# Optimization experiments

Hardware: AMD Instinct MI355X
Metric: run time of the kernel (lower is better)

The kernel has to match this reference:

```python
import jax, jax.numpy as jnp
import numpy as np

N_CON, N_VAR, E, D = 100000, 200000, 1600000, 128


def setup_inputs() -> dict:
    key = jax.random.key(0)
    ks = jax.random.split(key, 10)
    s = 1.0 / np.sqrt(D)
    return {
        "x_con": jax.random.normal(ks[0], (N_CON, D), jnp.float32),
        "x_var": jax.random.normal(ks[1], (N_VAR, D), jnp.float32),
        "e_con": jax.random.randint(ks[2], (E,), 0, N_CON, jnp.int32),
        "e_var": jax.random.randint(ks[3], (E,), 0, N_VAR, jnp.int32),
        # GraphConv for edge type constraint->variable (updates variable nodes)
        "W_rel_cv": jax.random.normal(ks[4], (D, D), jnp.float32) * s,
        "b_cv": jnp.zeros((D,), jnp.float32),
        "W_root_cv": jax.random.normal(ks[5], (D, D), jnp.float32) * s,
        # GraphConv for edge type variable->constraint (updates constraint nodes)
        "W_rel_vc": jax.random.normal(ks[6], (D, D), jnp.float32) * s,
        "b_vc": jnp.zeros((D,), jnp.float32),
        "W_root_vc": jax.random.normal(ks[7], (D, D), jnp.float32) * s,
        # per-node-type LayerNorm params
        "ln_g_con": jnp.ones((D,), jnp.float32),
        "ln_b_con": jnp.zeros((D,), jnp.float32),
        "ln_g_var": jnp.ones((D,), jnp.float32),
        "ln_b_var": jnp.zeros((D,), jnp.float32),
    }


def _layer_norm(x, g, b, eps=1e-5):
    m = jnp.mean(x, axis=-1, keepdims=True)
    v = jnp.var(x, axis=-1, keepdims=True)
    return (x - m) * jax.lax.rsqrt(v + eps) * g + b


def reference(x_con, x_var, e_con, e_var,
              W_rel_cv, b_cv, W_root_cv,
              W_rel_vc, b_vc, W_root_vc,
              ln_g_con, ln_b_con, ln_g_var, ln_b_var):
    # GraphConv (aggr='add'): out = lin_rel(sum_j x_j) + lin_root(x_dst)
    # constraint -> variable: gather constraint feats, scatter-add onto variables
    agg_var = jax.ops.segment_sum(x_con[e_con], e_var, num_segments=N_VAR)  # [N_VAR, D]
    out_var = agg_var @ W_rel_cv + b_cv + x_var @ W_root_cv
    # variable -> constraint (reverse edges)
    agg_con = jax.ops.segment_sum(x_var[e_var], e_con, num_segments=N_CON)  # [N_CON, D]
    out_con = agg_con @ W_rel_vc + b_vc + x_con @ W_root_vc
    # LayerNorm + ReLU per node type
    out_con = jax.nn.relu(_layer_norm(out_con, ln_g_con, ln_b_con))
    out_var = jax.nn.relu(_layer_norm(out_var, ln_g_var, ln_b_var))
    return out_con, out_var
```

## Files before the change

### kernel.cpp

```cpp
#include <hip/hip_runtime.h>
#include <hip/hip_bf16.h>
#include <hip/hip_fp16.h>

#define DD 128

typedef __attribute__((ext_vector_type(8))) short bf8;
typedef __attribute__((ext_vector_type(4))) float f32x4;

__device__ __forceinline__ ushort f2bf(float x) {
    return __bfloat16_as_ushort(__float2bfloat16(x));
}
__device__ __forceinline__ float bf2f(ushort h) {
    return __uint_as_float(((unsigned)h) << 16);
}

__global__ __launch_bounds__(256)
void to_fp16(const float* __restrict__ in, __half* __restrict__ out, long n)
{
    long i = ((long)blockIdx.x * 256 + threadIdx.x) * 8;
    if (i >= n) return;
    float4 a = *(const float4*)(in + i);
    float4 b = *(const float4*)(in + i + 4);
    __half2 h0 = __floats2half2_rn(a.x, a.y);
    __half2 h1 = __floats2half2_rn(a.z, a.w);
    __half2 h2 = __floats2half2_rn(b.x, b.y);
    __half2 h3 = __floats2half2_rn(b.z, b.w);
    uint4 o;
    o.x = *(unsigned*)&h0; o.y = *(unsigned*)&h1;
    o.z = *(unsigned*)&h2; o.w = *(unsigned*)&h3;
    *(uint4*)(out + i) = o;
}

#define NBMAX 640
#define CAP 16384

__global__ __launch_bounds__(256)
void bucket_hist(const int* __restrict__ e_con, const int* __restrict__ e_var,
                 int* __restrict__ btot, int N_CON, int NT, int E)
{
    __shared__ int cnt[NBMAX];
    const int NB = (NT + 511) >> 9;
    const int tid = threadIdx.x;
    for (int b = tid; b < NB; b += 256) cnt[b] = 0;
    __syncthreads();
    long e0 = (long)blockIdx.x * 4096;
#pragma unroll
    for (int i = 0; i < 16; ++i) {
        long e = e0 + i * 256 + tid;
        if (e < E) {
            atomicAdd(&cnt[e_con[e] >> 9], 1);
            atomicAdd(&cnt[(N_CON + e_var[e]) >> 9], 1);
        }
    }
    __syncthreads();
    for (int b = tid; b < NB; b += 256)
        if (cnt[b]) atomicAdd(&btot[b], cnt[b]);
}

__global__ __launch_bounds__(1024)
void bucket_scan(const int* __restrict__ btot, int* __restrict__ gbase,
                 int* __restrict__ gcursor, int NB)
{
    const int tid = threadIdx.x, lane = tid & 63, wave = tid >> 6;
    int v = (tid < NB) ? btot[tid] : 0;
    int x = v;
#pragma unroll
    for (int d = 1; d < 64; d <<= 1) {
        int y = __shfl_up(x, d);
        if (lane >= d) x += y;
    }
    __shared__ int wt[16];
    if (lane == 63) wt[wave] = x;
    __syncthreads();
    int off = 0;
    for (int w = 0; w < wave; ++w) off += wt[w];
    int excl = x - v + off;
    if (tid < NB) { gbase[tid] = excl; gcursor[tid] = excl; }
    if (tid == NB - 1) gbase[NB] = excl + v;
}

__global__ __launch_bounds__(256)
void binA(const int* __restrict__ e_con, const int* __restrict__ e_var,
          int* __restrict__ gcursor, unsigned* __restrict__ staging,
          int N_CON, int NT, int E)
{
    __shared__ int cnt[NBMAX], base[NBMAX];
    const int NB = (NT + 511) >> 9;
    const int tid = threadIdx.x;
    for (int b = tid; b < NB; b += 256) cnt[b] = 0;
    __syncthreads();
    long e0 = (long)blockIdx.x * 4096;
    int cs[16], vs[16];
#pragma unroll
    for (int i = 0; i < 16; ++i) {
        long e = e0 + i * 256 + tid;
        bool ok = e < E;
        cs[i] = ok ? e_con[e] : -1;
        vs[i] = ok ? e_var[e] : 0;
    }
#pragma unroll
    for (int i = 0; i < 16; ++i) if (cs[i] >= 0) {
        atomicAdd(&cnt[cs[i] >> 9], 1);
        atomicAdd(&cnt[(N_CON + vs[i]) >> 9], 1);
    }
    __syncthreads();
    for (int b = tid; b < NB; b += 256) {
        int c = cnt[b];
        base[b] = c ? atomicAdd(&gcursor[b], c) : 0;
        cnt[b] = 0;
    }
    __syncthreads();
#pragma unroll
    for (int i = 0; i < 16; ++i) if (cs[i] >= 0) {
        int d1 = cs[i];
        int p1 = base[d1 >> 9] + atomicAdd(&cnt[d1 >> 9], 1);
        staging[p1] = ((unsigned)(d1 & 511) << 18) | (unsigned)vs[i];
        int d2 = N_CON + vs[i];
        int p2 = base[d2 >> 9] + atomicAdd(&cnt[d2 >> 9], 1);
        staging[p2] = ((unsigned)(d2 & 511) << 18) | (unsigned)cs[i];
    }
}

__global__ __launch_bounds__(256)
void bucket_sort(const unsigned* __restrict__ staging, const int* __restrict__ gbase,
                 int* __restrict__ row_ptr, int* __restrict__ srclist, int NT)
{
    __shared__ int dcnt[512], dbase[512], wt[4];
    __shared__ unsigned srcbuf[CAP];
    const int b = blockIdx.x, tid = threadIdx.x;
    const int nbase = gbase[b];
    int n = gbase[b + 1] - nbase;
    if (n > CAP) n = CAP;

    for (int i = tid; i < 512; i += 256) dcnt[i] = 0;
    __syncthreads();
    for (int i = tid; i < n; i += 256)
        atomicAdd(&dcnt[staging[nbase + i] >> 18], 1);
    __syncthreads();

    int c0 = dcnt[2 * tid], c1 = dcnt[2 * tid + 1];
    int ts = c0 + c1, x = ts;
#pragma unroll
    for (int d = 1; d < 64; d <<= 1) {
        int y = __shfl_up(x, d);
        if ((tid & 63) >= d) x += y;
    }
    if ((tid & 63) == 63) wt[tid >> 6] = x;
    __syncthreads();
    int woff = 0;
    for (int w = 0; w < (tid >> 6); ++w) woff += wt[w];
    int ex = x - ts + woff;
    dbase[2 * tid] = ex;
    dbase[2 * tid + 1] = ex + c0;
    int nd = (b << 9) + 2 * tid;
    if (nd < NT)     row_ptr[nd]     = nbase + ex;
    if (nd + 1 < NT) row_ptr[nd + 1] = nbase + ex + c0;
    __syncthreads();

    for (int i = tid; i < 512; i += 256) dcnt[i] = 0;
    __syncthreads();
    for (int i = tid; i < n; i += 256) {
        unsigned e = staging[nbase + i];
        int d = e >> 18;
        int pos = dbase[d] + atomicAdd(&dcnt[d], 1);
        srcbuf[pos] = e & 0x3FFFFu;
    }
    __syncthreads();
    for (int i = tid; i < n; i += 256)
        srclist[nbase + i] = (int)srcbuf[i];
}

__global__ __launch_bounds__(256)
void gather_kernel(const __half2* __restrict__ hc, const __half2* __restrict__ hv,
                   const int* __restrict__ row_ptr, const int* __restrict__ srclist,
                   float* __restrict__ out, int N_CON, int NT, int twoE)
{
    int n = blockIdx.x * 4 + (threadIdx.x >> 6);
    if (n >= NT) return;
    int lane = threadIdx.x & 63;
    int start = row_ptr[n];
    int end = (n + 1 < NT) ? row_ptr[n + 1] : twoE;
    const __half2* src = (n < N_CON) ? hv : hc;

    float2 a0 = make_float2(0.f, 0.f);
    float2 a1 = make_float2(0.f, 0.f);
    int j = start;
    for (; j + 8 <= end; j += 8) {
        int i0 = srclist[j + 0], i1 = srclist[j + 1];
        int i2 = srclist[j + 2], i3 = srclist[j + 3];
        int i4 = srclist[j + 4], i5 = srclist[j + 5];
        int i6 = srclist[j + 6], i7 = srclist[j + 7];
        float2 t0 = __half22float2(src[(long)i0 * 64 + lane]);
        float2 t1 = __half22float2(src[(long)i1 * 64 + lane]);
        float2 t2 = __half22float2(src[(long)i2 * 64 + lane]);
        float2 t3 = __half22float2(src[(long)i3 * 64 + lane]);
        float2 t4 = __half22float2(src[(long)i4 * 64 + lane]);
        float2 t5 = __half22float2(src[(long)i5 * 64 + lane]);
        float2 t6 = __half22float2(src[(long)i6 * 64 + lane]);
        float2 t7 = __half22float2(src[(long)i7 * 64 + lane]);
        a0.x += (t0.x + t1.x) + (t2.x + t3.x);
        a0.y += (t0.y + t1.y) + (t2.y + t3.y);
        a1.x += (t4.x + t5.x) + (t6.x + t7.x);
        a1.y += (t4.y + t5.y) + (t6.y + t7.y);
    }
    if (j + 4 <= end) {
        int i0 = srclist[j + 0], i1 = srclist[j + 1];
        int i2 = srclist[j + 2], i3 = srclist[j + 3];
        float2 t0 = __half22float2(src[(long)i0 * 64 + lane]);
        float2 t1 = __half22float2(src[(long)i1 * 64 + lane]);
        float2 t2 = __half22float2(src[(long)i2 * 64 + lane]);
        float2 t3 = __half22float2(src[(long)i3 * 64 + lane]);
        a0.x += (t0.x + t1.x) + (t2.x + t3.x);
        a0.y += (t0.y + t1.y) + (t2.y + t3.y);
        j += 4;
    }
    if (j + 2 <= end) {
        int i0 = srclist[j + 0], i1 = srclist[j + 1];
        float2 t0 = __half22float2(src[(long)i0 * 64 + lane]);
        float2 t1 = __half22float2(src[(long)i1 * 64 + lane]);
        a1.x += t0.x + t1.x;
        a1.y += t0.y + t1.y;
        j += 2;
    }
    if (j < end) {
        float2 t0 = __half22float2(src[(long)srclist[j] * 64 + lane]);
        a0.x += t0.x;
        a0.y += t0.y;
    }
    a0.x += a1.x; a0.y += a1.y;
    ((float2*)(out + (long)n * DD))[lane] = a0;
}

__global__ __launch_bounds__(512, 4)
void gemm_mfma_ln(const float* __restrict__ agg, const float* __restrict__ xroot,
                  const float* __restrict__ Wrel, const float* __restrict__ Wroot,
                  const float* __restrict__ bias,
                  const float* __restrict__ ln_g, const float* __restrict__ ln_b,
                  float* __restrict__ out, int M)
{
    __shared__ ushort Blds[2 * 8192];

    const int wid  = threadIdx.x >> 6;
    const int lane = threadIdx.x & 63;
    const int lq   = lane >> 4;
    const int lc   = lane & 15;
    const long wrow0 = (long)blockIdx.x * 256 + wid * 32;

    const float* ap[2]; const float* xp[2];
#pragma unroll
    for (int rt = 0; rt < 2; ++rt) {
        long rr = wrow0 + rt * 16 + lc;
        if (rr >= M) rr = 0;
        ap[rt] = agg   + rr * DD;
        xp[rt] = xroot + rr * DD;
    }

    f32x4 acc[2][8] = {};

    for (int c = 0; c < 4; ++c) {
        const float* W = (c < 2) ? Wrel : Wroot;
        const int krow0 = (c & 1) * 8;
        __syncthreads();
        for (int g = threadIdx.x; g < 1024; g += 512) {
            int krl = g >> 7, col = g & 127;
            const float* wp = W + (long)(krow0 + krl) * 8 * DD + col;
            bf8 vh, vl;
#pragma unroll
            for (int j = 0; j < 8; ++j) {
                float w = wp[(long)j * DD];
                ushort h = f2bf(w);
                vh[j] = (short)h;
                vl[j] = (short)f2bf(w - bf2f(h));
            }
            int base = (g * 8) ^ ((krl & 3) << 3);
            *(bf8*)&Blds[base] = vh;
            *(bf8*)&Blds[8192 + base] = vl;
        }
        __syncthreads();

#pragma unroll
        for (int ks2 = 0; ks2 < 2; ++ks2) {
            const int ks = c * 2 + ks2;
            const int kk0 = ks * 32;
            bf8 ah[2], al[2];
#pragma unroll
            for (int rt = 0; rt < 2; ++rt) {
                const float* rp = (ks < 4) ? ap[rt] : xp[rt];
                const int koff  = (ks < 4) ? kk0 : (kk0 - 128);
                const float4* p = (const float4*)(rp + koff + lq * 8);
                float4 f0 = p[0], f1 = p[1];
                float v[8] = {f0.x, f0.y, f0.z, f0.w, f1.x, f1.y, f1.z, f1.w};
#pragma unroll
                for (int j = 0; j < 8; ++j) {
                    ushort h = f2bf(v[j]);
                    ah[rt][j] = (short)h;
                    al[rt][j] = (short)f2bf(v[j] - bf2f(h));
                }
            }
            const int krl0 = ks2 * 4 + lq;
#pragma unroll
            for (int colt = 0; colt < 8; ++colt) {
                int off = ((krl0 * 128 + colt * 16 + lc) * 8) ^ (lq << 3);
                bf8 bh = *(const bf8*)&Blds[off];
                bf8 bl = *(const bf8*)&Blds[8192 + off];
#pragma unroll
                for (int rt = 0; rt < 2; ++rt) {
                    acc[rt][colt] = __builtin_amdgcn_mfma_f32_16x16x32_bf16(ah[rt], bh, acc[rt][colt], 0, 0, 0);
                    acc[rt][colt] = __builtin_amdgcn_mfma_f32_16x16x32_bf16(ah[rt], bl, acc[rt][colt], 0, 0, 0);
                    acc[rt][colt] = __builtin_amdgcn_mfma_f32_16x16x32_bf16(al[rt], bh, acc[rt][colt], 0, 0, 0);
                }
            }
        }
    }

    float biasv[8], gv[8], bv[8];
#pragma unroll
    for (int colt = 0; colt < 8; ++colt) {
        int col = colt * 16 + lc;
        biasv[colt] = bias[col]; gv[colt] = ln_g[col]; bv[colt] = ln_b[col];
    }
#pragma unroll
    for (int rt = 0; rt < 2; ++rt) {
#pragma unroll
        for (int r = 0; r < 4; ++r) {
            long row = wrow0 + rt * 16 + lq * 4 + r;
            float v[8];
            float s = 0.f;
#pragma unroll
            for (int colt = 0; colt < 8; ++colt) { v[colt] = acc[rt][colt][r] + biasv[colt]; s += v[colt]; }
#pragma unroll
            for (int m = 8; m >= 1; m >>= 1) s += __shfl_xor(s, m);
            float mean = s * (1.0f / 128.0f);
            float vq = 0.f;
#pragma unroll
            for (int colt = 0; colt < 8; ++colt) { v[colt] -= mean; vq += v[colt] * v[colt]; }
#pragma unroll
            for (int m = 8; m >= 1; m >>= 1) vq += __shfl_xor(vq, m);
            float inv = rsqrtf(vq * (1.0f / 128.0f) + 1e-5f);
            if (row < M) {
#pragma unroll
                for (int colt = 0; colt < 8; ++colt) {
                    out[row * DD + colt * 16 + lc] =
                        fmaxf(fmaf(v[colt] * inv, gv[colt], bv[colt]), 0.f);
                }
            }
        }
    }
}

extern "C" void kernel_launch(void* const* d_in, const int* in_sizes, int n_in,
                              void* d_out, int out_size, void* d_ws, size_t ws_size,
                              hipStream_t stream)
{
    const float* x_con     = (const float*)d_in[0];
    const float* x_var     = (const float*)d_in[1];
    const int*   e_con     = (const int*)d_in[2];
    const int*   e_var     = (const int*)d_in[3];
    const float* W_rel_cv  = (const float*)d_in[4];
    const float* b_cv      = (const float*)d_in[5];
    const float* W_root_cv = (const float*)d_in[6];
    const float* W_rel_vc  = (const float*)d_in[7];
    const float* b_vc      = (const float*)d_in[8];
    const float* W_root_vc = (const float*)d_in[9];
    const float* ln_g_con  = (const float*)d_in[10];
    const float* ln_b_con  = (const float*)d_in[11];
    const float* ln_g_var  = (const float*)d_in[12];
    const float* ln_b_var  = (const float*)d_in[13];

    const int N_CON = in_sizes[0] / DD;
    const int N_VAR = in_sizes[1] / DD;
    const int E     = in_sizes[2];
    const int NT    = N_CON + N_VAR;
    const int twoE  = 2 * E;
    const int NB    = (NT + 511) >> 9;

    __half*   hxc     = (__half*)d_ws;
    __half*   hxv     = hxc + (size_t)N_CON * DD;
    int*      row_ptr = (int*)(hxv + (size_t)N_VAR * DD);
    int*      srclist = row_ptr + NT;
    unsigned* staging = (unsigned*)(srclist + twoE);
    int*      btot    = (int*)(staging + twoE);
    int*      gbase   = btot + NB;
    int*      gcursor = gbase + NB + 1;

    float* out_all = (float*)d_out;

    const int eb4 = (E + 4095) / 4096;
    const long nc_elems = (long)N_CON * DD, nv_elems = (long)N_VAR * DD;

    hipMemsetAsync(btot, 0, (size_t)NB * sizeof(int), stream);
    to_fp16<<<(int)((nc_elems / 8 + 255) / 256), 256, 0, stream>>>(x_con, hxc, nc_elems);
    to_fp16<<<(int)((nv_elems / 8 + 255) / 256), 256, 0, stream>>>(x_var, hxv, nv_elems);
    bucket_hist<<<eb4, 256, 0, stream>>>(e_con, e_var, btot, N_CON, NT, E);
    bucket_scan<<<1, 1024, 0, stream>>>(btot, gbase, gcursor, NB);
    binA<<<eb4, 256, 0, stream>>>(e_con, e_var, gcursor, staging, N_CON, NT, E);
    bucket_sort<<<NB, 256, 0, stream>>>(staging, gbase, row_ptr, srclist, NT);

    gather_kernel<<<(NT + 3) / 4, 256, 0, stream>>>((const __half2*)hxc, (const __half2*)hxv,
                                                    row_ptr, srclist,
                                                    out_all, N_CON, NT, twoE);

    gemm_mfma_ln<<<(N_CON + 255) / 256, 512, 0, stream>>>(
        out_all, x_con, W_rel_vc, W_root_vc, b_vc, ln_g_con, ln_b_con, out_all, N_CON);
    gemm_mfma_ln<<<(N_VAR + 255) / 256, 512, 0, stream>>>(
        out_all + (size_t)N_CON * DD, x_var, W_rel_cv, W_root_cv, b_cv,
        ln_g_var, ln_b_var, out_all + (size_t)N_CON * DD, N_VAR);
}
```

Measured before the change: 390.9 us.

## Drop histogram pass via fixed-capacity buckets; store aggregates as split bf16

Binning now writes edges into fixed-capacity per-bucket staging slots using a global cursor, so the separate histogram kernel goes away and the prefix scan runs after binning on the final counts. The gather kernel writes each aggregated row as pre-split bf16 high/low halves instead of fp32, so the GEMM loads MFMA operands directly and skips the conversion for the aggregate half of K. The staging buffer grows to NB*CAPS entries, and edges beyond the bucket capacity are dropped silently, which matches the existing clamp in bucket_sort.

```diff
diff --git a/kernel.cpp b/kernel.cpp
--- a/kernel.cpp
+++ b/kernel.cpp
@@ -3,6 +3,8 @@
 #include <hip/hip_fp16.h>
 
 #define DD 128
+#define CAPS 16384
+#define NBMAX 640
 
 typedef __attribute__((ext_vector_type(8))) short bf8;
 typedef __attribute__((ext_vector_type(4))) float f32x4;
@@ -31,53 +33,6 @@
     *(uint4*)(out + i) = o;
 }
 
-#define NBMAX 640
-#define CAP 16384
-
-__global__ __launch_bounds__(256)
-void bucket_hist(const int* __restrict__ e_con, const int* __restrict__ e_var,
-                 int* __restrict__ btot, int N_CON, int NT, int E)
-{
-    __shared__ int cnt[NBMAX];
-    const int NB = (NT + 511) >> 9;
-    const int tid = threadIdx.x;
-    for (int b = tid; b < NB; b += 256) cnt[b] = 0;
-    __syncthreads();
-    long e0 = (long)blockIdx.x * 4096;
-#pragma unroll
-    for (int i = 0; i < 16; ++i) {
-        long e = e0 + i * 256 + tid;
-        if (e < E) {
-            atomicAdd(&cnt[e_con[e] >> 9], 1);
-            atomicAdd(&cnt[(N_CON + e_var[e]) >> 9], 1);
-        }
-    }
-    __syncthreads();
-    for (int b = tid; b < NB; b += 256)
-        if (cnt[b]) atomicAdd(&btot[b], cnt[b]);
-}
-
-__global__ __launch_bounds__(1024)
-void bucket_scan(const int* __restrict__ btot, int* __restrict__ gbase,
-                 int* __restrict__ gcursor, int NB)
-{
-    const int tid = threadIdx.x, lane = tid & 63, wave = tid >> 6;
-    int v = (tid < NB) ? btot[tid] : 0;
-    int x = v;
-#pragma unroll
-    for (int d = 1; d < 64; d <<= 1) {
-        int y = __shfl_up(x, d);
-        if (lane >= d) x += y;
-    }
-    __shared__ int wt[16];
-    if (lane == 63) wt[wave] = x;
-    __syncthreads();
-    int off = 0;
-    for (int w = 0; w < wave; ++w) off += wt[w];
-    int excl = x - v + off;
-    if (tid < NB) { gbase[tid] = excl; gcursor[tid] = excl; }
-    if (tid == NB - 1) gbase[NB] = excl + v;
-}
 
 __global__ __launch_bounds__(256)
 void binA(const int* __restrict__ e_con, const int* __restrict__ e_var,
@@ -112,13 +67,36 @@
     __syncthreads();
 #pragma unroll
     for (int i = 0; i < 16; ++i) if (cs[i] >= 0) {
-        int d1 = cs[i];
-        int p1 = base[d1 >> 9] + atomicAdd(&cnt[d1 >> 9], 1);
-        staging[p1] = ((unsigned)(d1 & 511) << 18) | (unsigned)vs[i];
-        int d2 = N_CON + vs[i];
-        int p2 = base[d2 >> 9] + atomicAdd(&cnt[d2 >> 9], 1);
-        staging[p2] = ((unsigned)(d2 & 511) << 18) | (unsigned)cs[i];
-    }
+        int d1 = cs[i], b1 = d1 >> 9;
+        int p1 = base[b1] + atomicAdd(&cnt[b1], 1);
+        if (p1 < CAPS)
+            staging[(long)b1 * CAPS + p1] = ((unsigned)(d1 & 511) << 18) | (unsigned)vs[i];
+        int d2 = N_CON + vs[i], b2 = d2 >> 9;
+        int p2 = base[b2] + atomicAdd(&cnt[b2], 1);
+        if (p2 < CAPS)
+            staging[(long)b2 * CAPS + p2] = ((unsigned)(d2 & 511) << 18) | (unsigned)cs[i];
+    }
+}
+
+__global__ __launch_bounds__(1024)
+void bucket_scan(const int* __restrict__ btot, int* __restrict__ gbase, int NB)
+{
+    const int tid = threadIdx.x, lane = tid & 63, wave = tid >> 6;
+    int v = (tid < NB) ? btot[tid] : 0;
+    int x = v;
+#pragma unroll
+    for (int d = 1; d < 64; d <<= 1) {
+        int y = __shfl_up(x, d);
+        if (lane >= d) x += y;
+    }
+    __shared__ int wt[16];
+    if (lane == 63) wt[wave] = x;
+    __syncthreads();
+    int off = 0;
+    for (int w = 0; w < wave; ++w) off += wt[w];
+    int excl = x - v + off;
+    if (tid < NB) gbase[tid] = excl;
+    if (tid == NB - 1) gbase[NB] = excl + v;
 }
 
 __global__ __launch_bounds__(256)
@@ -126,16 +104,17 @@
                  int* __restrict__ row_ptr, int* __restrict__ srclist, int NT)
 {
     __shared__ int dcnt[512], dbase[512], wt[4];
-    __shared__ unsigned srcbuf[CAP];
+    __shared__ unsigned srcbuf[CAPS];
     const int b = blockIdx.x, tid = threadIdx.x;
     const int nbase = gbase[b];
     int n = gbase[b + 1] - nbase;
-    if (n > CAP) n = CAP;
+    if (n > CAPS) n = CAPS;
+    const unsigned* st = staging + (long)b * CAPS;
 
     for (int i = tid; i < 512; i += 256) dcnt[i] = 0;
     __syncthreads();
     for (int i = tid; i < n; i += 256)
-        atomicAdd(&dcnt[staging[nbase + i] >> 18], 1);
+        atomicAdd(&dcnt[st[i] >> 18], 1);
     __syncthreads();
 
     int c0 = dcnt[2 * tid], c1 = dcnt[2 * tid + 1];
@@ -160,7 +139,7 @@
     for (int i = tid; i < 512; i += 256) dcnt[i] = 0;
     __syncthreads();
     for (int i = tid; i < n; i += 256) {
-        unsigned e = staging[nbase + i];
+        unsigned e = st[i];
         int d = e >> 18;
         int pos = dbase[d] + atomicAdd(&dcnt[d], 1);
         srcbuf[pos] = e & 0x3FFFFu;
@@ -227,8 +206,12 @@
         a0.x += t0.x;
         a0.y += t0.y;
     }
-    a0.x += a1.x; a0.y += a1.y;
-    ((float2*)(out + (long)n * DD))[lane] = a0;
+    float s0 = a0.x + a1.x, s1 = a0.y + a1.y;
+    ushort h0 = f2bf(s0), h1 = f2bf(s1);
+    ushort l0 = f2bf(s0 - bf2f(h0)), l1 = f2bf(s1 - bf2f(h1));
+    char* rowb = (char*)(out + (long)n * DD);
+    *(unsigned*)(rowb + 4 * lane)       = (unsigned)h0 | ((unsigned)h1 << 16);
+    *(unsigned*)(rowb + 256 + 4 * lane) = (unsigned)l0 | ((unsigned)l1 << 16);
 }
 
 __global__ __launch_bounds__(512, 4)
@@ -246,13 +229,13 @@
     const int lc   = lane & 15;
     const long wrow0 = (long)blockIdx.x * 256 + wid * 32;
 
-    const float* ap[2]; const float* xp[2];
+    const char*  apb[2]; const float* xp[2];
 #pragma unroll
     for (int rt = 0; rt < 2; ++rt) {
         long rr = wrow0 + rt * 16 + lc;
         if (rr >= M) rr = 0;
-        ap[rt] = agg   + rr * DD;
-        xp[rt] = xroot + rr * DD;
+        apb[rt] = (const char*)(agg + rr * DD);
+        xp[rt]  = xroot + rr * DD;
     }
 
     f32x4 acc[2][8] = {};
@@ -283,18 +266,25 @@
             const int ks = c * 2 + ks2;
             const int kk0 = ks * 32;
             bf8 ah[2], al[2];
-#pragma unroll
-            for (int rt = 0; rt < 2; ++rt) {
-                const float* rp = (ks < 4) ? ap[rt] : xp[rt];
-                const int koff  = (ks < 4) ? kk0 : (kk0 - 128);
-                const float4* p = (const float4*)(rp + koff + lq * 8);
-                float4 f0 = p[0], f1 = p[1];
-                float v[8] = {f0.x, f0.y, f0.z, f0.w, f1.x, f1.y, f1.z, f1.w};
-#pragma unroll
-                for (int j = 0; j < 8; ++j) {
-                    ushort h = f2bf(v[j]);
-                    ah[rt][j] = (short)h;
-                    al[rt][j] = (short)f2bf(v[j] - bf2f(h));
+            if (c < 2) {
+#pragma unroll
+                for (int rt = 0; rt < 2; ++rt) {
+                    int boff = (kk0 + lq * 8) * 2;
+                    ah[rt] = *(const bf8*)(apb[rt] + boff);
+                    al[rt] = *(const bf8*)(apb[rt] + 256 + boff);
+                }
+            } else {
+#pragma unroll
+                for (int rt = 0; rt < 2; ++rt) {
+                    const float4* p = (const float4*)(xp[rt] + (kk0 - 128) + lq * 8);
+                    float4 f0 = p[0], f1 = p[1];
+                    float v[8] = {f0.x, f0.y, f0.z, f0.w, f1.x, f1.y, f1.z, f1.w};
+#pragma unroll
+                    for (int j = 0; j < 8; ++j) {
+                        ushort h = f2bf(v[j]);
+                        ah[rt][j] = (short)h;
+                        al[rt][j] = (short)f2bf(v[j] - bf2f(h));
+                    }
                 }
             }
             const int krl0 = ks2 * 4 + lq;
@@ -379,21 +369,19 @@
     int*      row_ptr = (int*)(hxv + (size_t)N_VAR * DD);
     int*      srclist = row_ptr + NT;
     unsigned* staging = (unsigned*)(srclist + twoE);
-    int*      btot    = (int*)(staging + twoE);
-    int*      gbase   = btot + NB;
-    int*      gcursor = gbase + NB + 1;
+    int*      gcursor = (int*)(staging + (size_t)NB * CAPS);
+    int*      gbase   = gcursor + NB;
 
     float* out_all = (float*)d_out;
 
     const int eb4 = (E + 4095) / 4096;
     const long nc_elems = (long)N_CON * DD, nv_elems = (long)N_VAR * DD;
 
-    hipMemsetAsync(btot, 0, (size_t)NB * sizeof(int), stream);
+    hipMemsetAsync(gcursor, 0, (size_t)NB * sizeof(int), stream);
     to_fp16<<<(int)((nc_elems / 8 + 255) / 256), 256, 0, stream>>>(x_con, hxc, nc_elems);
     to_fp16<<<(int)((nv_elems / 8 + 255) / 256), 256, 0, stream>>>(x_var, hxv, nv_elems);
-    bucket_hist<<<eb4, 256, 0, stream>>>(e_con, e_var, btot, N_CON, NT, E);
-    bucket_scan<<<1, 1024, 0, stream>>>(btot, gbase, gcursor, NB);
     binA<<<eb4, 256, 0, stream>>>(e_con, e_var, gcursor, staging, N_CON, NT, E);
+    bucket_scan<<<1, 1024, 0, stream>>>(gcursor, gbase, NB);
     bucket_sort<<<NB, 256, 0, stream>>>(staging, gbase, row_ptr, srclist, NT);
 
     gather_kernel<<<(NT + 3) / 4, 256, 0, stream>>>((const __half2*)hxc, (const __half2*)hxv,
```

After: 363.9 us. 1.07x faster.
